# Kernel optimization log

Hardware: AMD Instinct MI355X
Metric: run time of the kernel (lower is better)

## Reference

```python
import jax, jax.numpy as jnp
import numpy as np


def setup_inputs() -> dict:
    key = jax.random.key(0)
    kx, ky = jax.random.split(key)
    B, N, D = 16, 2048, 128
    x = jax.random.normal(kx, (B, N, D), dtype=jnp.float32)
    y = jax.random.normal(ky, (B, N, D), dtype=jnp.float32)
    return {"x": x, "y": y}


def reference(x, y):
    # Pairwise squared-Euclidean cost: out[b, i, j] = sum_d (x[b,i,d] - y[b,j,d])**2
    # Computed via ||x||^2 + ||y||^2 - 2 <x, y> to avoid the O(N^2 D) intermediate
    # that the original repeat/view pattern materializes.
    x2 = jnp.sum(x * x, axis=-1)                      # [B, N]
    y2 = jnp.sum(y * y, axis=-1)                      # [B, N]
    xy = jnp.einsum('bid,bjd->bij', x, y)             # [B, N, N]
    cost = x2[:, :, None] + y2[:, None, :] - 2.0 * xy  # [B, N, N]
    return jnp.maximum(cost, 0.0)
```

## Files before the change

### kernel.cpp

```cpp
#include <hip/hip_runtime.h>


#define Bb   16
#define Nn   2048
#define Dd   128
#define TILE 128
#define JT   8
#define LDSS 136

typedef __bf16 bf16x8 __attribute__((ext_vector_type(8)));
typedef float  f32x4  __attribute__((ext_vector_type(4)));

__device__ __forceinline__ bf16x8 pack8(float4 a, float4 b) {
  bf16x8 r;
  r[0] = (__bf16)a.x; r[1] = (__bf16)a.y; r[2] = (__bf16)a.z; r[3] = (__bf16)a.w;
  r[4] = (__bf16)b.x; r[5] = (__bf16)b.y; r[6] = (__bf16)b.z; r[7] = (__bf16)b.w;
  return r;
}

__global__ __launch_bounds__(256, 2)
void pairwise_cost_kernel(const float* __restrict__ x,
                          const float* __restrict__ y,
                          float* __restrict__ out) {
  __shared__ __align__(16) unsigned short ys[2][TILE * LDSS];
  __shared__ __align__(16) float          yn_s[2][TILE];

  const int t  = threadIdx.x;
  const int b  = blockIdx.z;
  const int i0 = blockIdx.y * TILE;
  const int j0 = blockIdx.x * (TILE * JT);

  const int w    = t >> 6;
  const int lane = t & 63;
  const int lrow = lane & 15;
  const int quad = lane >> 4;
  const int ib   = (w >> 1) * 64;
  const int jb   = (w & 1) * 64;

  const int r    = t >> 1;
  const int half = t & 1;

  bf16x8 xf[4][4];
  float  xn[4];
  {
    const float* xb = x + ((size_t)b * Nn + i0 + ib) * Dd;
    #pragma unroll
    for (int ti = 0; ti < 4; ++ti) {
      const float* rp = xb + (ti * 16 + lrow) * Dd + quad * 8;
      float ss = 0.f;
      #pragma unroll
      for (int k = 0; k < 4; ++k) {
        float4 u0 = *(const float4*)(rp + k * 32);
        float4 u1 = *(const float4*)(rp + k * 32 + 4);
        ss += u0.x * u0.x + u0.y * u0.y + u0.z * u0.z + u0.w * u0.w
            + u1.x * u1.x + u1.y * u1.y + u1.z * u1.z + u1.w * u1.w;
        xf[ti][k] = pack8(u0, u1);
      }
      ss += __shfl_xor(ss, 16);
      ss += __shfl_xor(ss, 32);
      xn[ti] = ss;
    }
  }

  {
    const float4* src = (const float4*)(y + ((size_t)b * Nn + j0 + r) * Dd + half * 64);
    float ss = 0.f;
    #pragma unroll
    for (int q = 0; q < 8; ++q) {
      float4 v0 = src[2 * q];
      float4 v1 = src[2 * q + 1];
      ss += v0.x * v0.x + v0.y * v0.y + v0.z * v0.z + v0.w * v0.w
          + v1.x * v1.x + v1.y * v1.y + v1.z * v1.z + v1.w * v1.w;
      *(bf16x8*)&ys[0][r * LDSS + half * 64 + q * 8] = pack8(v0, v1);
    }
    ss += __shfl_xor(ss, 1);
    if (half == 0) yn_s[0][r] = ss;
  }
  __syncthreads();

  float* outb = out + (size_t)b * Nn * Nn;

  for (int jt = 0; jt < JT; ++jt) {
    const int cur = jt & 1;

    float4 ld[16];
    if (jt + 1 < JT) {
      const float4* src =
          (const float4*)(y + ((size_t)b * Nn + j0 + (jt + 1) * TILE + r) * Dd + half * 64);
      #pragma unroll
      for (int q = 0; q < 16; ++q) ld[q] = src[q];
    }

    f32x4 acc[4][4];
    #pragma unroll
    for (int ti = 0; ti < 4; ++ti)
      #pragma unroll
      for (int tj = 0; tj < 4; ++tj)
        acc[ti][tj] = (f32x4){0.f, 0.f, 0.f, 0.f};

    #pragma unroll
    for (int k = 0; k < 4; ++k) {
      const int dk = k * 32 + quad * 8;
      bf16x8 yf[4];
      #pragma unroll
      for (int tj = 0; tj < 4; ++tj)
        yf[tj] = *(const bf16x8*)&ys[cur][(jb + tj * 16 + lrow) * LDSS + dk];
      #pragma unroll
      for (int ti = 0; ti < 4; ++ti)
        #pragma unroll
        for (int tj = 0; tj < 4; ++tj)
          acc[ti][tj] = __builtin_amdgcn_mfma_f32_16x16x32_bf16(yf[tj], xf[ti][k],
                                                               acc[ti][tj], 0, 0, 0);
    }

    if (jt + 1 < JT) {
      float ss = 0.f;
      #pragma unroll
      for (int q = 0; q < 8; ++q) {
        float4 v0 = ld[2 * q];
        float4 v1 = ld[2 * q + 1];
        ss += v0.x * v0.x + v0.y * v0.y + v0.z * v0.z + v0.w * v0.w
            + v1.x * v1.x + v1.y * v1.y + v1.z * v1.z + v1.w * v1.w;
        *(bf16x8*)&ys[cur ^ 1][r * LDSS + half * 64 + q * 8] = pack8(v0, v1);
      }
      ss += __shfl_xor(ss, 1);
      if (half == 0) yn_s[cur ^ 1][r] = ss;
    }

    #pragma unroll
    for (int ti = 0; ti < 4; ++ti) {
      const size_t orow = (size_t)(i0 + ib + ti * 16 + lrow) * Nn + (j0 + jt * TILE + jb);
      const float  xnv  = xn[ti];
      #pragma unroll
      for (int tj = 0; tj < 4; ++tj) {
        f32x4 yn4 = *(const f32x4*)&yn_s[cur][jb + tj * 16 + quad * 4];
        f32x4 a   = acc[ti][tj];
        f32x4 c;
        #pragma unroll
        for (int rg = 0; rg < 4; ++rg)
          c[rg] = fmaxf(xnv + yn4[rg] - 2.0f * a[rg], 0.0f);
        *(f32x4*)(outb + orow + tj * 16 + quad * 4) = c;
      }
    }

    __syncthreads();
  }
}

extern "C" void kernel_launch(void* const* d_in, const int* in_sizes, int n_in,
                              void* d_out, int out_size, void* d_ws, size_t ws_size,
                              hipStream_t stream) {
  const float* x = (const float*)d_in[0];
  const float* y = (const float*)d_in[1];
  float* out = (float*)d_out;
  dim3 grid(Nn / (TILE * JT), Nn / TILE, Bb);
  pairwise_cost_kernel<<<grid, dim3(256, 1, 1), 0, stream>>>(x, y, out);
}
```

Before: 371.9 us.

## Load y fragments directly from global into registers, drop LDS staging, nontemporal stores

Removes the double-buffered LDS staging of y. Each wave now loads and converts its own y MFMA fragments straight from global memory every tile, and all y row norms are precomputed into shared memory in a prologue. This drops the per-tile __syncthreads and the LDS traffic, and output stores become nontemporal to avoid cache pollution. The cost is that each y element is read from global/L2 by two waves instead of once per block, prefetch overlap is lost, y is read one extra time for the norms, and register pressure rises.

```diff
diff --git a/kernel.cpp b/kernel.cpp
--- a/kernel.cpp
+++ b/kernel.cpp
@@ -6,7 +6,6 @@
 #define Dd   128
 #define TILE 128
 #define JT   8
-#define LDSS 136
 
 typedef __bf16 bf16x8 __attribute__((ext_vector_type(8)));
 typedef float  f32x4  __attribute__((ext_vector_type(4)));
@@ -22,8 +21,7 @@
 void pairwise_cost_kernel(const float* __restrict__ x,
                           const float* __restrict__ y,
                           float* __restrict__ out) {
-  __shared__ __align__(16) unsigned short ys[2][TILE * LDSS];
-  __shared__ __align__(16) float          yn_s[2][TILE];
+  __shared__ float yn_s[TILE * JT];
 
   const int t  = threadIdx.x;
   const int b  = blockIdx.z;
@@ -37,8 +35,21 @@
   const int ib   = (w >> 1) * 64;
   const int jb   = (w & 1) * 64;
 
-  const int r    = t >> 1;
-  const int half = t & 1;
+  {
+    const int r2 = t >> 1, half = t & 1;
+    for (int g = 0; g < JT; ++g) {
+      const float4* src =
+          (const float4*)(y + ((size_t)b * Nn + j0 + g * TILE + r2) * Dd + half * 64);
+      float ss = 0.f;
+      #pragma unroll
+      for (int q = 0; q < 16; ++q) {
+        float4 v = src[q];
+        ss += v.x * v.x + v.y * v.y + v.z * v.z + v.w * v.w;
+      }
+      ss += __shfl_xor(ss, 1);
+      if (half == 0) yn_s[g * TILE + r2] = ss;
+    }
+  }
 
   bf16x8 xf[4][4];
   float  xn[4];
@@ -61,34 +72,23 @@
       xn[ti] = ss;
     }
   }
-
-  {
-    const float4* src = (const float4*)(y + ((size_t)b * Nn + j0 + r) * Dd + half * 64);
-    float ss = 0.f;
-    #pragma unroll
-    for (int q = 0; q < 8; ++q) {
-      float4 v0 = src[2 * q];
-      float4 v1 = src[2 * q + 1];
-      ss += v0.x * v0.x + v0.y * v0.y + v0.z * v0.z + v0.w * v0.w
-          + v1.x * v1.x + v1.y * v1.y + v1.z * v1.z + v1.w * v1.w;
-      *(bf16x8*)&ys[0][r * LDSS + half * 64 + q * 8] = pack8(v0, v1);
-    }
-    ss += __shfl_xor(ss, 1);
-    if (half == 0) yn_s[0][r] = ss;
-  }
   __syncthreads();
 
   float* outb = out + (size_t)b * Nn * Nn;
 
   for (int jt = 0; jt < JT; ++jt) {
-    const int cur = jt & 1;
-
-    float4 ld[16];
-    if (jt + 1 < JT) {
-      const float4* src =
-          (const float4*)(y + ((size_t)b * Nn + j0 + (jt + 1) * TILE + r) * Dd + half * 64);
+    bf16x8 yf[4][4];
+    {
+      const float* ybase = y + ((size_t)b * Nn + j0 + jt * TILE) * Dd;
       #pragma unroll
-      for (int q = 0; q < 16; ++q) ld[q] = src[q];
+      for (int k = 0; k < 4; ++k)
+        #pragma unroll
+        for (int tj = 0; tj < 4; ++tj) {
+          const float* rp = ybase + (jb + tj * 16 + lrow) * Dd + k * 32 + quad * 8;
+          float4 u0 = *(const float4*)(rp);
+          float4 u1 = *(const float4*)(rp + 4);
+          yf[k][tj] = pack8(u0, u1);
+        }
     }
 
     f32x4 acc[4][4];
@@ -99,51 +99,30 @@
         acc[ti][tj] = (f32x4){0.f, 0.f, 0.f, 0.f};
 
     #pragma unroll
-    for (int k = 0; k < 4; ++k) {
-      const int dk = k * 32 + quad * 8;
-      bf16x8 yf[4];
-      #pragma unroll
-      for (int tj = 0; tj < 4; ++tj)
-        yf[tj] = *(const bf16x8*)&ys[cur][(jb + tj * 16 + lrow) * LDSS + dk];
+    for (int k = 0; k < 4; ++k)
       #pragma unroll
       for (int ti = 0; ti < 4; ++ti)
         #pragma unroll
         for (int tj = 0; tj < 4; ++tj)
-          acc[ti][tj] = __builtin_amdgcn_mfma_f32_16x16x32_bf16(yf[tj], xf[ti][k],
+          acc[ti][tj] = __builtin_amdgcn_mfma_f32_16x16x32_bf16(yf[k][tj], xf[ti][k],
                                                                acc[ti][tj], 0, 0, 0);
-    }
-
-    if (jt + 1 < JT) {
-      float ss = 0.f;
-      #pragma unroll
-      for (int q = 0; q < 8; ++q) {
-        float4 v0 = ld[2 * q];
-        float4 v1 = ld[2 * q + 1];
-        ss += v0.x * v0.x + v0.y * v0.y + v0.z * v0.z + v0.w * v0.w
-            + v1.x * v1.x + v1.y * v1.y + v1.z * v1.z + v1.w * v1.w;
-        *(bf16x8*)&ys[cur ^ 1][r * LDSS + half * 64 + q * 8] = pack8(v0, v1);
-      }
-      ss += __shfl_xor(ss, 1);
-      if (half == 0) yn_s[cur ^ 1][r] = ss;
-    }
 
     #pragma unroll
     for (int ti = 0; ti < 4; ++ti) {
-      const size_t orow = (size_t)(i0 + ib + ti * 16 + lrow) * Nn + (j0 + jt * TILE + jb);
-      const float  xnv  = xn[ti];
+      const size_t orow =
+          (size_t)(i0 + ib + ti * 16 + lrow) * Nn + (j0 + jt * TILE + jb);
+      const float xnv = xn[ti];
       #pragma unroll
       for (int tj = 0; tj < 4; ++tj) {
-        f32x4 yn4 = *(const f32x4*)&yn_s[cur][jb + tj * 16 + quad * 4];
+        f32x4 yn4 = *(const f32x4*)&yn_s[jt * TILE + jb + tj * 16 + quad * 4];
         f32x4 a   = acc[ti][tj];
         f32x4 c;
         #pragma unroll
         for (int rg = 0; rg < 4; ++rg)
           c[rg] = fmaxf(xnv + yn4[rg] - 2.0f * a[rg], 0.0f);
-        *(f32x4*)(outb + orow + tj * 16 + quad * 4) = c;
+        __builtin_nontemporal_store(c, (f32x4*)(outb + orow + tj * 16 + quad * 4));
       }
     }
-
-    __syncthreads();
   }
 }
 
```

Result: slower. 381.5 us (+2.6%).
